# Performance work log

Measured on AMD Instinct MI355X. Metric: run time of the kernel, lower is better.

Reference implementation:

```python
import jax, jax.numpy as jnp
import numpy as np

DIM = 192
NUM_HEADS = 8
EPS = 1e-12  # torch F.normalize default eps


def setup_inputs() -> dict:
    key = jax.random.key(0)
    k1, k2, k3, k4 = jax.random.split(key, 4)
    b, c, h, w = 8, DIM, 128, 128
    x = jax.random.normal(k1, (b, c, h, w), dtype=jnp.float32)
    # 1x1 qkv conv weight, stored as (3c, c)
    w_qkv = jax.random.normal(k2, (3 * c, c), dtype=jnp.float32) * (1.0 / np.sqrt(c))
    # depthwise 3x3 conv weight, groups = 3c -> OIHW (3c, 1, 3, 3)
    w_dw = jax.random.normal(k3, (3 * c, 1, 3, 3), dtype=jnp.float32) * (1.0 / 3.0)
    # 1x1 project_out weight (c, c)
    w_out = jax.random.normal(k4, (c, c), dtype=jnp.float32) * (1.0 / np.sqrt(c))
    temperature = jnp.ones((NUM_HEADS, 1, 1), dtype=jnp.float32)
    return {"x": x, "w_qkv": w_qkv, "w_dw": w_dw, "w_out": w_out,
            "temperature": temperature}


def _mdta(x, w_qkv, w_dw, w_out, temperature):
    b, c, h, w = x.shape
    nh = NUM_HEADS
    # 1x1 conv == channel GEMM
    qkv = jnp.einsum('oc,bchw->bohw', w_qkv, x)
    # depthwise 3x3 conv, groups = 3c
    qkv = jax.lax.conv_general_dilated(
        qkv, w_dw, window_strides=(1, 1), padding='SAME',
        feature_group_count=3 * c,
        dimension_numbers=('NCHW', 'OIHW', 'NCHW'))
    q, k, v = jnp.split(qkv, 3, axis=1)
    hd = c // nh
    q = q.reshape(b, nh, hd, h * w)
    k = k.reshape(b, nh, hd, h * w)
    v = v.reshape(b, nh, hd, h * w)
    # L2 normalize over spatial (hw) dim
    q = q / jnp.maximum(jnp.linalg.norm(q, axis=-1, keepdims=True), EPS)
    k = k / jnp.maximum(jnp.linalg.norm(k, axis=-1, keepdims=True), EPS)
    # channel x channel attention per head: (b, nh, hd, hd)
    attn = jnp.einsum('bhcn,bhdn->bhcd', q, k) * temperature
    attn = jax.nn.softmax(attn, axis=-1)
    out = jnp.einsum('bhcd,bhdn->bhcn', attn, v).reshape(b, c, h, w)
    return jnp.einsum('oc,bchw->bohw', w_out, out)


def reference(x, w_qkv, w_dw, w_out, temperature):
    return _mdta(x, w_qkv, w_dw, w_out, temperature)
```

## Files before the change

kernel.cpp:

```cpp
#include <hip/hip_runtime.h>


#define HW 16384
#define WIMG 128
#define C 192
#define C3 576
#define NH 8
#define HD 24

typedef unsigned short ushort8_t __attribute__((ext_vector_type(8)));
typedef unsigned short ushort4_t __attribute__((ext_vector_type(4)));
typedef short short8_t __attribute__((ext_vector_type(8)));
typedef float float4_t __attribute__((ext_vector_type(4)));

__device__ __forceinline__ float bfu2f(unsigned short u) {
    union { unsigned int i; float f; } v; v.i = ((unsigned int)u) << 16; return v.f;
}
__device__ __forceinline__ unsigned short f2bfu(float f) {
    union { float f; unsigned int i; } v; v.f = f;
    unsigned int x = v.i;
    return (unsigned short)((x + 0x7FFFu + ((x >> 16) & 1u)) >> 16);
}
__device__ __forceinline__ float inload(const void* p, int idx, int isbf) {
    return isbf ? bfu2f(((const unsigned short*)p)[idx]) : ((const float*)p)[idx];
}

__device__ __forceinline__ int afrag_idx(int o, int dg) {
    return ((((o >> 4) * 6 + (dg >> 5)) * 4 + ((dg >> 3) & 3)) << 7)
           + ((o & 15) << 3) + (dg & 7);
}

__global__ void probe_dtype(const unsigned int* __restrict__ x, int* __restrict__ flag) {
    const int t = threadIdx.x;
    int cnt = 0;
    for (int i = t; i < 512; i += 256) {
        const unsigned int u = x[i] & 0xFFFFu;
        const unsigned int e = (u >> 7) & 0xFFu;
        if (u == 0u || (e >= 100u && e <= 140u)) cnt++;
    }
#pragma unroll
    for (int off = 32; off; off >>= 1) cnt += __shfl_down(cnt, off, 64);
    __shared__ int s[4];
    if ((t & 63) == 0) s[t >> 6] = cnt;
    __syncthreads();
    if (t == 0) flag[0] = (s[0] + s[1] + s[2] + s[3] > 300) ? 1 : 0;
}

__global__ void prep(const void* __restrict__ wqkv, const void* __restrict__ wdw,
                     const void* __restrict__ wout, const void* __restrict__ temp,
                     const int* __restrict__ flagp, unsigned short* __restrict__ wqb,
                     float* __restrict__ wdwf, float* __restrict__ woutf,
                     float* __restrict__ tempf, float* __restrict__ normsum) {
    const int isbf = flagp[0];
    const int id = blockIdx.x * 256 + threadIdx.x;
    const int stride = gridDim.x * 256;
    for (int i = id; i < C3 * C; i += stride) {
        const int o = i / C, dg = i - o * C;
        const unsigned short v =
            isbf ? ((const unsigned short*)wqkv)[i] : f2bfu(((const float*)wqkv)[i]);
        wqb[afrag_idx(o, dg)] = v;
    }
    for (int i = id; i < C3 * 9; i += stride) wdwf[i] = inload(wdw, i, isbf);
    for (int i = id; i < C * C; i += stride) woutf[i] = inload(wout, i, isbf);
    for (int i = id; i < NH; i += stride) tempf[i] = inload(temp, i, isbf);
    for (int i = id; i < 8 * 2 * C; i += stride) normsum[i] = 0.f;
}

__global__ __launch_bounds__(512) void gemm_mfma(
    const void* __restrict__ Bsrc, const unsigned short* __restrict__ Abf,
    void* __restrict__ outp, const int* __restrict__ flagp,
    size_t b_batch_stride, size_t b_const_off, size_t o_batch_stride,
    int a_batch_stride, int m_tiles, int b_mode, int out_mode) {
    __shared__ unsigned short sbuf[16384];
    const int isbf = flagp[0];
    const int b_isbf = b_mode | isbf;
    const int tid = threadIdx.x;
    const int batch = blockIdx.y;
    const int n0 = blockIdx.x * 128;
    const size_t b_off = b_batch_stride * batch + b_const_off;
    const size_t o_off = o_batch_stride * batch;
    const unsigned short* Ab = Abf + (size_t)a_batch_stride * batch;

    const int w = tid >> 6;
    const int lane = tid & 63;
    const int l15 = lane & 15;
    const int quad = lane >> 4;
    const int mhalf = w & 1;
    const int nquad = w >> 1;

    short8_t bfr[6][2];
#pragma unroll
    for (int h = 0; h < 2; h++) {
        if (h) __syncthreads();
        if (tid < 192) {
            const int cg = tid >> 4;
            const int pg = tid & 15;
            const int chbase = h * 96 + cg * 8;
            ushort8_t rows[8];
            if (b_isbf) {
                const unsigned short* bp = (const unsigned short*)Bsrc + b_off + n0 + pg * 8;
#pragma unroll
                for (int r = 0; r < 8; r++)
                    rows[r] = *reinterpret_cast<const ushort8_t*>(bp + (size_t)(chbase + r) * HW);
            } else {
                const float* bp = (const float*)Bsrc + b_off + n0 + pg * 8;
#pragma unroll
                for (int r = 0; r < 8; r++) {
                    const float4_t f0 = *reinterpret_cast<const float4_t*>(bp + (size_t)(chbase + r) * HW);
                    const float4_t f1 = *reinterpret_cast<const float4_t*>(bp + (size_t)(chbase + r) * HW + 4);
#pragma unroll
                    for (int i = 0; i < 4; i++) { rows[r][i] = f2bfu(f0[i]); rows[r][i + 4] = f2bfu(f1[i]); }
                }
            }
#pragma unroll
            for (int s = 0; s < 8; s++) {
                ushort8_t outv;
#pragma unroll
                for (int r = 0; r < 8; r++) outv[r] = rows[r][s];
                const int p = pg * 8 + s;
                const int cidx = p * 16 + (cg ^ s);
                *reinterpret_cast<ushort8_t*>(&sbuf[cidx * 8]) = outv;
            }
        }
        __syncthreads();
#pragma unroll
        for (int ksl = 0; ksl < 3; ksl++) {
            const int ks = h * 3 + ksl;
            const int cgl = ks * 4 + quad - h * 12;
#pragma unroll
            for (int nt = 0; nt < 2; nt++) {
                const int p = nquad * 32 + nt * 16 + l15;
                const int cidx = p * 16 + (cgl ^ (p & 7));
                bfr[ks][nt] = *reinterpret_cast<const short8_t*>(&sbuf[cidx * 8]);
            }
        }
    }

    const int o_isbf = out_mode ? isbf : 1;
    const int rr = tid >> 3;
    const int kk = tid & 7;
    for (int mt0 = 0; mt0 < m_tiles; mt0++) {
        const int m0 = mt0 * 64;
        short8_t afr[2][6];
#pragma unroll
        for (int mt = 0; mt < 2; mt++) {
            const int tile = mt0 * 4 + mhalf * 2 + mt;
#pragma unroll
            for (int ks = 0; ks < 6; ks++)
                afr[mt][ks] = *reinterpret_cast<const short8_t*>(
                    Ab + (size_t)((((tile * 6 + ks) << 2) + quad) << 7) + (l15 << 3));
        }
        float4_t acc[2][2];
#pragma unroll
        for (int mt = 0; mt < 2; mt++)
#pragma unroll
            for (int nt = 0; nt < 2; nt++) {
                float4_t z = {0.f, 0.f, 0.f, 0.f};
                acc[mt][nt] = z;
            }
#pragma unroll
        for (int ks = 0; ks < 6; ks++)
#pragma unroll
            for (int mt = 0; mt < 2; mt++)
#pragma unroll
                for (int nt = 0; nt < 2; nt++)
                    acc[mt][nt] = __builtin_amdgcn_mfma_f32_16x16x32_bf16(
                        afr[mt][ks], bfr[ks][nt], acc[mt][nt], 0, 0, 0);
        if (out_mode == 0) {
#pragma unroll
            for (int mt = 0; mt < 2; mt++) {
                const int ch4 = (m0 >> 2) + (mhalf * 2 + mt) * 4 + quad;
#pragma unroll
                for (int nt = 0; nt < 2; nt++) {
                    const int px = n0 + nquad * 32 + nt * 16 + l15;
                    ushort4_t v;
#pragma unroll
                    for (int r = 0; r < 4; r++) v[r] = f2bfu(acc[mt][nt][r]);
                    *reinterpret_cast<ushort4_t*>(
                        (unsigned short*)outp + o_off + ((size_t)ch4 * HW + px) * 4) = v;
                }
            }
        } else if (o_isbf) {
            __syncthreads();
#pragma unroll
            for (int mt = 0; mt < 2; mt++) {
                const int row64 = (mhalf * 2 + mt) * 16 + quad * 4;
#pragma unroll
                for (int nt = 0; nt < 2; nt++) {
                    const int col = nquad * 32 + nt * 16 + l15;
#pragma unroll
                    for (int r = 0; r < 4; r++)
                        sbuf[(row64 + r) * 136 + col] = f2bfu(acc[mt][nt][r]);
                }
            }
            __syncthreads();
            const ushort8_t v0 = *reinterpret_cast<const ushort8_t*>(&sbuf[rr * 136 + kk * 16]);
            const ushort8_t v1 = *reinterpret_cast<const ushort8_t*>(&sbuf[rr * 136 + kk * 16 + 8]);
            unsigned short* op = (unsigned short*)outp + o_off + (size_t)(m0 + rr) * HW + n0 + kk * 16;
            *reinterpret_cast<ushort8_t*>(op) = v0;
            *reinterpret_cast<ushort8_t*>(op + 8) = v1;
        } else {
#pragma unroll
            for (int mt = 0; mt < 2; mt++) {
                const int row = m0 + (mhalf * 2 + mt) * 16 + quad * 4;
#pragma unroll
                for (int nt = 0; nt < 2; nt++) {
                    const int col = n0 + nquad * 32 + nt * 16 + l15;
#pragma unroll
                    for (int r = 0; r < 4; r++)
                        ((float*)outp)[o_off + (size_t)(row + r) * HW + col] = acc[mt][nt][r];
                }
            }
        }
    }
}

__global__ __launch_bounds__(256) void dwconv(
    const unsigned short* __restrict__ qkv0i, const float* __restrict__ wdwf,
    unsigned short* __restrict__ qkv1, float* __restrict__ normsum) {
    const int cg4 = blockIdx.y;
    const int b = blockIdx.z;
    const int t = threadIdx.x;
    const int wave = t >> 6, lane = t & 63;
    const int y = blockIdx.x * 4 + wave;
    const int px0 = lane * 2;
    const size_t ibase = ((size_t)b * 144 + cg4) * HW * 4;
    const float* wp = wdwf + cg4 * 36;

    float acc[4][2];
#pragma unroll
    for (int c = 0; c < 4; c++) { acc[c][0] = 0.f; acc[c][1] = 0.f; }

#pragma unroll
    for (int dy = 0; dy < 3; dy++) {
        const int yy = y + dy - 1;
        if (yy < 0 || yy > 127) continue;
        const ushort8_t m = *reinterpret_cast<const ushort8_t*>(
            qkv0i + ibase + (size_t)(yy * WIMG + px0) * 4);
        float fm0[4], fm1[4];
#pragma unroll
        for (int c = 0; c < 4; c++) { fm0[c] = bfu2f(m[c]); fm1[c] = bfu2f(m[4 + c]); }
#pragma unroll
        for (int c = 0; c < 4; c++) {
            float lf = __shfl_up(fm1[c], 1, 64);
            float rf = __shfl_down(fm0[c], 1, 64);
            if (lane == 0) lf = 0.f;
            if (lane == 63) rf = 0.f;
            const float w0 = wp[c * 9 + dy * 3], w1 = wp[c * 9 + dy * 3 + 1],
                        w2 = wp[c * 9 + dy * 3 + 2];
            acc[c][0] += w0 * lf + w1 * fm0[c] + w2 * fm1[c];
            acc[c][1] += w0 * fm0[c] + w1 * fm1[c] + w2 * rf;
        }
    }
#pragma unroll
    for (int c = 0; c < 4; c++) {
        const unsigned int pk =
            (unsigned int)f2bfu(acc[c][0]) | ((unsigned int)f2bfu(acc[c][1]) << 16);
        *reinterpret_cast<unsigned int*>(
            qkv1 + ((size_t)b * C3 + cg4 * 4 + c) * HW + y * WIMG + px0) = pk;
    }
    if (cg4 < 96) {
        float ss[4];
#pragma unroll
        for (int c = 0; c < 4; c++) ss[c] = acc[c][0] * acc[c][0] + acc[c][1] * acc[c][1];
#pragma unroll
        for (int off = 32; off; off >>= 1)
#pragma unroll
            for (int c = 0; c < 4; c++) ss[c] += __shfl_down(ss[c], off, 64);
        __shared__ float red[4][4];
        if (lane == 0)
#pragma unroll
            for (int c = 0; c < 4; c++) red[wave][c] = ss[c];
        __syncthreads();
        if (t < 4)
            atomicAdd(&normsum[b * 2 * C + cg4 * 4 + t],
                      red[0][t] + red[1][t] + red[2][t] + red[3][t]);
    }
}

#define AG_LROW 264
__global__ __launch_bounds__(256) void attn_gram(
    const unsigned short* __restrict__ qkv1, float* __restrict__ Spart) {
    __shared__ unsigned short qk[2 * 32 * AG_LROW];
    const int b = blockIdx.z, h = blockIdx.y;
    const int t = threadIdx.x;
    const size_t qbase0 = (size_t)b * C3 * HW + (size_t)(h * HD) * HW;
    const size_t kbase0 = qbase0 + (size_t)C * HW;
    const int wave = t >> 6, lane = t & 63;
    const int l15 = lane & 15, quad = lane >> 4;

    for (int s = t; s < 2 * 8 * 33; s += 256) {
        const int tt = s / (8 * 33);
        const int rm = s - tt * (8 * 33);
        const int row = 24 + rm / 33;
        const int c16 = rm % 33;
        ushort8_t z;
#pragma unroll
        for (int i = 0; i < 8; i++) z[i] = 0;
        *reinterpret_cast<ushort8_t*>(&qk[(tt * 32 + row) * AG_LROW + c16 * 8]) = z;
    }

    float4_t acc[2][2];
#pragma unroll
    for (int mt = 0; mt < 2; mt++)
#pragma unroll
        for (int nt = 0; nt < 2; nt++) {
            float4_t z = {0.f, 0.f, 0.f, 0.f};
            acc[mt][nt] = z;
        }

    for (int cc = 0; cc < 4; cc++) {
        const int k0 = (blockIdx.x * 4 + cc) * 256;
        __syncthreads();
#pragma unroll
        for (int it = 0; it < 6; it++) {
            const int s = it * 256 + t;
            const int tt = s >= 768;
            const int rm = s - tt * 768;
            const int row = rm >> 5;
            const int c16 = rm & 31;
            const ushort8_t v = *reinterpret_cast<const ushort8_t*>(
                qkv1 + (tt ? kbase0 : qbase0) + k0 + (size_t)row * HW + c16 * 8);
            *reinterpret_cast<ushort8_t*>(&qk[(tt * 32 + row) * AG_LROW + c16 * 8]) = v;
        }
        __syncthreads();
#pragma unroll
        for (int ks = 0; ks < 2; ks++) {
            const int kkk = wave * 64 + ks * 32 + quad * 8;
            short8_t qa[2], kb[2];
#pragma unroll
            for (int mt = 0; mt < 2; mt++)
                qa[mt] = *reinterpret_cast<const short8_t*>(
                    &qk[(mt * 16 + l15) * AG_LROW + kkk]);
#pragma unroll
            for (int nt = 0; nt < 2; nt++)
                kb[nt] = *reinterpret_cast<const short8_t*>(
                    &qk[(32 + nt * 16 + l15) * AG_LROW + kkk]);
#pragma unroll
            for (int mt = 0; mt < 2; mt++)
#pragma unroll
                for (int nt = 0; nt < 2; nt++)
                    acc[mt][nt] = __builtin_amdgcn_mfma_f32_16x16x32_bf16(
                        qa[mt], kb[nt], acc[mt][nt], 0, 0, 0);
        }
    }

    __syncthreads();
    float* fs = (float*)qk;
#pragma unroll
    for (int mt = 0; mt < 2; mt++)
#pragma unroll
        for (int nt = 0; nt < 2; nt++)
#pragma unroll
            for (int r = 0; r < 4; r++)
                fs[((mt * 2 + nt) * 4 + r) * 256 + t] = acc[mt][nt][r];
    __syncthreads();
    if (t < 64) {
        float* Sb = Spart + (((size_t)blockIdx.x * 8 + b) * 8 + h) * (HD * HD);
#pragma unroll
        for (int mt = 0; mt < 2; mt++)
#pragma unroll
            for (int nt = 0; nt < 2; nt++) {
                const int j = nt * 16 + l15;
#pragma unroll
                for (int r = 0; r < 4; r++) {
                    const int i = mt * 16 + quad * 4 + r;
                    const int q2 = (mt * 2 + nt) * 4 + r;
                    const float v = fs[q2 * 256 + t] + fs[q2 * 256 + 64 + t] +
                                    fs[q2 * 256 + 128 + t] + fs[q2 * 256 + 192 + t];
                    if (i < HD && j < HD) Sb[i * HD + j] = v;
                }
            }
    }
}

__global__ void buildM(const float* __restrict__ Spart, const float* __restrict__ normsum,
                       const float* __restrict__ tempf, const float* __restrict__ woutf,
                       unsigned short* __restrict__ Mb) {
    __shared__ float As[NH * HD * HD];
    __shared__ float inv[2 * C];
    const int b = blockIdx.y;
    const int tid = threadIdx.x;
    for (int r = tid; r < 2 * C; r += 256)
        inv[r] = 1.f / fmaxf(sqrtf(normsum[b * 2 * C + r]), 1e-12f);
    __syncthreads();
    for (int e = tid; e < NH * HD * HD; e += 256) {
        const int h = e / (HD * HD);
        const int rm = e - h * HD * HD;
        const int i = rm / HD, j = rm % HD;
        float s = 0.f;
#pragma unroll
        for (int sp = 0; sp < 16; sp++)
            s += Spart[(((size_t)sp * 8 + b) * 8 + h) * (HD * HD) + rm];
        As[e] = s * inv[h * HD + i] * inv[C + h * HD + j] * tempf[h];
    }
    __syncthreads();
    if (tid < C) {
        const int h = tid / HD, i = tid % HD;
        float* rp = As + h * HD * HD + i * HD;
        float mx = -1e30f;
#pragma unroll
        for (int j = 0; j < HD; j++) mx = fmaxf(mx, rp[j]);
        float sum = 0.f;
#pragma unroll
        for (int j = 0; j < HD; j++) { rp[j] = __expf(rp[j] - mx); sum += rp[j]; }
        const float is = 1.f / sum;
#pragma unroll
        for (int j = 0; j < HD; j++) rp[j] *= is;
    }
    __syncthreads();
    const int idx = blockIdx.x * 256 + tid;
    const int o = idx / C, dg = idx % C;
    const int h = dg / HD, d = dg % HD;
    const float* wp = woutf + o * C + h * HD;
    const float* Ap = As + h * HD * HD + d;
    float acc = 0.f;
#pragma unroll
    for (int c2 = 0; c2 < HD; c2++) acc += wp[c2] * Ap[c2 * HD];
    Mb[(size_t)b * C * C + afrag_idx(o, dg)] = f2bfu(acc);
}

extern "C" void kernel_launch(void* const* d_in, const int* in_sizes, int n_in,
                              void* d_out, int out_size, void* d_ws, size_t ws_size,
                              hipStream_t stream) {
    const void* x    = d_in[0];
    const void* wqkv = d_in[1];
    const void* wdw  = d_in[2];
    const void* wout = d_in[3];
    const void* temp = d_in[4];

    char* w = (char*)d_ws;
    int* flag = (int*)w;                          w += 64;
    unsigned short* wqb = (unsigned short*)w;     w += (size_t)C3 * C * 2;
    unsigned short* Mb  = (unsigned short*)w;     w += (size_t)8 * C * C * 2;
    float* wdwf  = (float*)w;                     w += (size_t)C3 * 9 * 4;
    float* woutf = (float*)w;                     w += (size_t)C * C * 4;
    float* tempf = (float*)w;                     w += 64;
    float* normsum = (float*)w;                   w += (size_t)8 * 2 * C * 4;
    float* Spart = (float*)w;                     w += (size_t)16 * 8 * NH * HD * HD * 4;
    unsigned short* qkv0 = (unsigned short*)w;    w += (size_t)8 * C3 * HW * 2;
    unsigned short* qkv1 = (unsigned short*)w;

    probe_dtype<<<1, 256, 0, stream>>>((const unsigned int*)x, flag);
    prep<<<432, 256, 0, stream>>>(wqkv, wdw, wout, temp, flag, wqb, wdwf, woutf,
                                  tempf, normsum);
    gemm_mfma<<<dim3(HW / 128, 8), 512, 0, stream>>>(
        x, wqb, qkv0, flag, (size_t)C * HW, 0, (size_t)C3 * HW, 0, 9, 0, 0);
    dwconv<<<dim3(32, 144, 8), 256, 0, stream>>>(qkv0, wdwf, qkv1, normsum);
    attn_gram<<<dim3(16, NH, 8), 256, 0, stream>>>(qkv1, Spart);
    buildM<<<dim3(144, 8), 256, 0, stream>>>(Spart, normsum, tempf, woutf, Mb);
    gemm_mfma<<<dim3(HW / 128, 8), 512, 0, stream>>>(
        qkv1, Mb, d_out, flag, (size_t)C3 * HW, (size_t)2 * C * HW, (size_t)C * HW,
        C * C, 3, 1, 1);
}
```

Baseline: 394.0 us.

## Store qkv intermediate row-major per image row and use packed bf16 conversion

```diff
diff --git a/kernel.cpp b/kernel.cpp
--- a/kernel.cpp
+++ b/kernel.cpp
@@ -12,6 +12,8 @@
 typedef unsigned short ushort4_t __attribute__((ext_vector_type(4)));
 typedef short short8_t __attribute__((ext_vector_type(8)));
 typedef float float4_t __attribute__((ext_vector_type(4)));
+typedef unsigned int uint4_t __attribute__((ext_vector_type(4)));
+typedef unsigned int uint2_t __attribute__((ext_vector_type(2)));
 
 __device__ __forceinline__ float bfu2f(unsigned short u) {
     union { unsigned int i; float f; } v; v.i = ((unsigned int)u) << 16; return v.f;
@@ -20,6 +22,17 @@
     union { float f; unsigned int i; } v; v.f = f;
     unsigned int x = v.i;
     return (unsigned short)((x + 0x7FFFu + ((x >> 16) & 1u)) >> 16);
+}
+__device__ __forceinline__ float lo2f(unsigned int u) {
+    union { unsigned int i; float f; } v; v.i = u << 16; return v.f;
+}
+__device__ __forceinline__ float hi2f(unsigned int u) {
+    union { unsigned int i; float f; } v; v.i = u & 0xFFFF0000u; return v.f;
+}
+__device__ __forceinline__ unsigned int cvtpk(float a, float b) {
+    unsigned int r;
+    asm("v_cvt_pk_bf16_f32 %0, %1, %2" : "=v"(r) : "v"(a), "v"(b));
+    return r;
 }
 __device__ __forceinline__ float inload(const void* p, int idx, int isbf) {
     return isbf ? bfu2f(((const unsigned short*)p)[idx]) : ((const float*)p)[idx];
@@ -139,6 +152,8 @@
     const int o_isbf = out_mode ? isbf : 1;
     const int rr = tid >> 3;
     const int kk = tid & 7;
+    unsigned short* obase0 =
+        (unsigned short*)outp + o_off + (size_t)blockIdx.x * (144 * 512);
     for (int mt0 = 0; mt0 < m_tiles; mt0++) {
         const int m0 = mt0 * 64;
         short8_t afr[2][6];
@@ -172,12 +187,11 @@
                 const int ch4 = (m0 >> 2) + (mhalf * 2 + mt) * 4 + quad;
 #pragma unroll
                 for (int nt = 0; nt < 2; nt++) {
-                    const int px = n0 + nquad * 32 + nt * 16 + l15;
-                    ushort4_t v;
-#pragma unroll
-                    for (int r = 0; r < 4; r++) v[r] = f2bfu(acc[mt][nt][r]);
-                    *reinterpret_cast<ushort4_t*>(
-                        (unsigned short*)outp + o_off + ((size_t)ch4 * HW + px) * 4) = v;
+                    const int pxl = nquad * 32 + nt * 16 + l15;
+                    uint2_t v;
+                    v[0] = cvtpk(acc[mt][nt][0], acc[mt][nt][1]);
+                    v[1] = cvtpk(acc[mt][nt][2], acc[mt][nt][3]);
+                    *reinterpret_cast<uint2_t*>(obase0 + (size_t)(ch4 * 128 + pxl) * 4) = v;
                 }
             }
         } else if (o_isbf) {
@@ -224,7 +238,6 @@
     const int wave = t >> 6, lane = t & 63;
     const int y = blockIdx.x * 4 + wave;
     const int px0 = lane * 2;
-    const size_t ibase = ((size_t)b * 144 + cg4) * HW * 4;
     const float* wp = wdwf + cg4 * 36;
 
     float acc[4][2];
@@ -235,27 +248,46 @@
     for (int dy = 0; dy < 3; dy++) {
         const int yy = y + dy - 1;
         if (yy < 0 || yy > 127) continue;
-        const ushort8_t m = *reinterpret_cast<const ushort8_t*>(
-            qkv0i + ibase + (size_t)(yy * WIMG + px0) * 4);
-        float fm0[4], fm1[4];
-#pragma unroll
-        for (int c = 0; c < 4; c++) { fm0[c] = bfu2f(m[c]); fm1[c] = bfu2f(m[4 + c]); }
-#pragma unroll
-        for (int c = 0; c < 4; c++) {
-            float lf = __shfl_up(fm1[c], 1, 64);
-            float rf = __shfl_down(fm0[c], 1, 64);
-            if (lane == 0) lf = 0.f;
-            if (lane == 63) rf = 0.f;
-            const float w0 = wp[c * 9 + dy * 3], w1 = wp[c * 9 + dy * 3 + 1],
-                        w2 = wp[c * 9 + dy * 3 + 2];
-            acc[c][0] += w0 * lf + w1 * fm0[c] + w2 * fm1[c];
-            acc[c][1] += w0 * fm0[c] + w1 * fm1[c] + w2 * rf;
+        const uint4_t mu = *reinterpret_cast<const uint4_t*>(
+            qkv0i + ((((size_t)b * 128 + yy) * 144 + cg4) << 9) + px0 * 4);
+        unsigned int lu01 = (unsigned int)__shfl_up((int)mu[2], 1, 64);
+        unsigned int lu23 = (unsigned int)__shfl_up((int)mu[3], 1, 64);
+        unsigned int ru01 = (unsigned int)__shfl_down((int)mu[0], 1, 64);
+        unsigned int ru23 = (unsigned int)__shfl_down((int)mu[1], 1, 64);
+        if (lane == 0)  { lu01 = 0u; lu23 = 0u; }
+        if (lane == 63) { ru01 = 0u; ru23 = 0u; }
+        const float w00 = wp[0 * 9 + dy * 3], w01 = wp[0 * 9 + dy * 3 + 1], w02 = wp[0 * 9 + dy * 3 + 2];
+        const float w10 = wp[1 * 9 + dy * 3], w11 = wp[1 * 9 + dy * 3 + 1], w12 = wp[1 * 9 + dy * 3 + 2];
+        const float w20 = wp[2 * 9 + dy * 3], w21 = wp[2 * 9 + dy * 3 + 1], w22 = wp[2 * 9 + dy * 3 + 2];
+        const float w30 = wp[3 * 9 + dy * 3], w31 = wp[3 * 9 + dy * 3 + 1], w32 = wp[3 * 9 + dy * 3 + 2];
+        {
+            const float fm0 = lo2f(mu[0]), fm1 = lo2f(mu[2]);
+            const float lf = lo2f(lu01), rf = lo2f(ru01);
+            acc[0][0] += w00 * lf + w01 * fm0 + w02 * fm1;
+            acc[0][1] += w00 * fm0 + w01 * fm1 + w02 * rf;
+        }
+        {
+            const float fm0 = hi2f(mu[0]), fm1 = hi2f(mu[2]);
+            const float lf = hi2f(lu01), rf = hi2f(ru01);
+            acc[1][0] += w10 * lf + w11 * fm0 + w12 * fm1;
+            acc[1][1] += w10 * fm0 + w11 * fm1 + w12 * rf;
+        }
+        {
+            const float fm0 = lo2f(mu[1]), fm1 = lo2f(mu[3]);
+            const float lf = lo2f(lu23), rf = lo2f(ru23);
+            acc[2][0] += w20 * lf + w21 * fm0 + w22 * fm1;
+            acc[2][1] += w20 * fm0 + w21 * fm1 + w22 * rf;
+        }
+        {
+            const float fm0 = hi2f(mu[1]), fm1 = hi2f(mu[3]);
+            const float lf = hi2f(lu23), rf = hi2f(ru23);
+            acc[3][0] += w30 * lf + w31 * fm0 + w32 * fm1;
+            acc[3][1] += w30 * fm0 + w31 * fm1 + w32 * rf;
         }
     }
 #pragma unroll
     for (int c = 0; c < 4; c++) {
-        const unsigned int pk =
-            (unsigned int)f2bfu(acc[c][0]) | ((unsigned int)f2bfu(acc[c][1]) << 16);
+        const unsigned int pk = cvtpk(acc[c][0], acc[c][1]);
         *reinterpret_cast<unsigned int*>(
             qkv1 + ((size_t)b * C3 + cg4 * 4 + c) * HW + y * WIMG + px0) = pk;
     }
```

Result: no change. 391.0 us (-0.8%).
